# Kernel tuning notes

Hardware: AMD Instinct MI355X
Metric: run time of the kernel (lower is better)

## Reference

```python
import jax, jax.numpy as jnp
import numpy as np

VOCAB = 100000
BEO = 512
BATCH = 2048
SEQ = 50
MEAN = 0.0
STD = 1.0


def _linear_params(key, fan_in, fan_out):
    k1, k2 = jax.random.split(key)
    bound = 1.0 / np.sqrt(fan_in)
    W = jax.random.uniform(k1, (fan_in, fan_out), jnp.float32, -bound, bound)
    b = jax.random.uniform(k2, (fan_out,), jnp.float32, -bound, bound)
    return W, b


def setup_inputs() -> dict:
    key = jax.random.key(0)
    ks = jax.random.split(key, 8)
    s = jax.random.randint(ks[0], (BATCH, SEQ), 0, VOCAB, dtype=jnp.int64)
    x = jax.random.normal(ks[1], (BATCH, BEO), dtype=jnp.float32)
    W_bow_h, b_bow_h = _linear_params(ks[2], VOCAB, 256)
    W_bow_pred, b_bow_pred = _linear_params(ks[3], 256, 5)
    W_bow_embd, b_bow_embd = _linear_params(ks[4], 256, 64)
    W_beo_h, b_beo_h = _linear_params(ks[5], BEO, 256)
    W_beo_pred, b_beo_pred = _linear_params(ks[6], 256, 5)
    W_beo_embd, b_beo_embd = _linear_params(ks[7], 256, 64)
    return {
        "s": s, "x": x,
        "W_bow_h": W_bow_h, "b_bow_h": b_bow_h,
        "W_bow_pred": W_bow_pred, "b_bow_pred": b_bow_pred,
        "W_bow_embd": W_bow_embd, "b_bow_embd": b_bow_embd,
        "W_beo_h": W_beo_h, "b_beo_h": b_beo_h,
        "W_beo_pred": W_beo_pred, "b_beo_pred": b_beo_pred,
        "W_beo_embd": W_beo_embd, "b_beo_embd": b_beo_embd,
    }


def reference(s, x,
              W_bow_h, b_bow_h, W_bow_pred, b_bow_pred, W_bow_embd, b_bow_embd,
              W_beo_h, b_beo_h, W_beo_pred, b_beo_pred, W_beo_embd, b_beo_embd):
    B = s.shape[0]
    xn = (x - MEAN) / STD
    # multi-hot: scatter_ sets 1 regardless of duplicates (set, not add)
    rows = jnp.arange(B)[:, None]  # [B,1] broadcasts against s [B,SEQ]
    bow = jnp.zeros((B, VOCAB), jnp.float32).at[rows, s].set(1.0)
    bow_h = jax.nn.leaky_relu(bow @ W_bow_h + b_bow_h, 0.2)  # [B,256]
    beo_h = jax.nn.leaky_relu(xn @ W_beo_h + b_beo_h, 0.2)   # [B,256]
    bow_p = bow_h @ W_bow_pred + b_bow_pred  # [B,5]
    beo_p = beo_h @ W_beo_pred + b_beo_pred  # [B,5]
    bow_e = bow_h @ W_bow_embd + b_bow_embd  # [B,64]
    beo_e = beo_h @ W_beo_embd + b_beo_embd  # [B,64]
    return (bow_e, beo_e, bow_p, beo_p)
```

## Files before the change

### kernel.cpp

```cpp
#include <hip/hip_runtime.h>
#include <cstdint>

#define VOCAB 100000
#define NB    2048
#define SEQ   50
#define HID   256
#define XIN   512
#define NE    64
#define NP    5

#define BEO_BLOCKS 256
#define BEO_ROWS   8
#define NBLK (BEO_BLOCKS + NB)

#define OFF_BOW_E 0
#define OFF_BEO_E (NB*NE)
#define OFF_BOW_P (2*NB*NE)
#define OFF_BEO_P (2*NB*NE + NB*NP)

#define GITER 13

struct BeoS { float xs[BEO_ROWS][XIN]; };
struct BowS { float part[4*HID]; float h[HID]; };
union  SMem { BeoS beo; BowS bow; };

__global__ __launch_bounds__(256, 1) void fused_kernel(
    const int*   __restrict__ s,   const float* __restrict__ x,
    const float* __restrict__ Wbh, const float* __restrict__ bbh,
    const float* __restrict__ Wbp, const float* __restrict__ bbp,
    const float* __restrict__ Wbe, const float* __restrict__ bbe,
    const float* __restrict__ Weh, const float* __restrict__ beh,
    const float* __restrict__ Wep, const float* __restrict__ bep,
    const float* __restrict__ Wee, const float* __restrict__ bee,
    float* __restrict__ out)
{
    __shared__ SMem sm;
    const int tid = threadIdx.x;
    const int blk = blockIdx.x;

    if (blk < BEO_BLOCKS) {
        const int r0 = blk * BEO_ROWS;
        {
            const float4* src = (const float4*)(x + (size_t)r0 * XIN);
            float4*       dst = (float4*)&sm.beo.xs[0][0];
            #pragma unroll
            for (int i = 0; i < (BEO_ROWS*XIN/4)/256; ++i)
                dst[i*256 + tid] = src[i*256 + tid];
        }
        __syncthreads();

        float acc[BEO_ROWS];
        {
            float bv = beh[tid];
            #pragma unroll
            for (int r = 0; r < BEO_ROWS; ++r) acc[r] = bv;
        }
        const float4* xs4 = (const float4*)&sm.beo.xs[0][0];
        #pragma unroll 2
        for (int k4 = 0; k4 < XIN/4; ++k4) {
            const float* wcol = Weh + (size_t)(4*k4)*HID + tid;
            float w0 = wcol[0];
            float w1 = wcol[HID];
            float w2 = wcol[2*HID];
            float w3 = wcol[3*HID];
            #pragma unroll
            for (int r = 0; r < BEO_ROWS; ++r) {
                float4 xv = xs4[r*(XIN/4) + k4];
                acc[r] = fmaf(xv.x, w0, acc[r]);
                acc[r] = fmaf(xv.y, w1, acc[r]);
                acc[r] = fmaf(xv.z, w2, acc[r]);
                acc[r] = fmaf(xv.w, w3, acc[r]);
            }
        }
        __syncthreads();
        float* hs = &sm.beo.xs[0][0];
        #pragma unroll
        for (int r = 0; r < BEO_ROWS; ++r) {
            float v = acc[r];
            hs[r*HID + tid] = v > 0.f ? v : 0.2f*v;
        }
        __syncthreads();

        {
            const int jj = tid & 63;
            const int r  = tid >> 6;
            const float4* hs4 = (const float4*)hs;
            float s0 = 0.f, s1 = 0.f;
            #pragma unroll 4
            for (int k4 = 0; k4 < HID/4; ++k4) {
                float4 ha = hs4[r*(HID/4) + k4];
                float4 hb = hs4[(r+4)*(HID/4) + k4];
                const float* wp = Wee + (size_t)(4*k4)*NE + jj;
                float w0 = wp[0], w1 = wp[NE], w2 = wp[2*NE], w3 = wp[3*NE];
                s0 = fmaf(ha.x, w0, s0); s0 = fmaf(ha.y, w1, s0);
                s0 = fmaf(ha.z, w2, s0); s0 = fmaf(ha.w, w3, s0);
                s1 = fmaf(hb.x, w0, s1); s1 = fmaf(hb.y, w1, s1);
                s1 = fmaf(hb.z, w2, s1); s1 = fmaf(hb.w, w3, s1);
            }
            float bias = bee[jj];
            out[OFF_BEO_E + (size_t)(r0+r)*NE   + jj] = s0 + bias;
            out[OFF_BEO_E + (size_t)(r0+r+4)*NE + jj] = s1 + bias;
        }
        if (tid < BEO_ROWS*NP) {
            const int r = tid / NP, jj = tid % NP;
            float sp = bep[jj];
            for (int k = 0; k < HID; ++k)
                sp = fmaf(hs[r*HID + k], Wep[k*NP + jj], sp);
            out[OFF_BEO_P + (size_t)(r0+r)*NP + jj] = sp;
        }
    } else {
        const int row  = blk - BEO_BLOCKS;
        const int lane = tid & 63;
        const int w    = tid >> 6;
        const int* srow = s + row * SEQ;

        int tokl = (lane < SEQ) ? srow[lane] : -3;

        int   tk[GITER];
        float mk[GITER];
        #pragma unroll
        for (int ii = 0; ii < GITER; ++ii) {
            const int i = w + 4*ii;
            int t = (i < SEQ) ? srow[i] : -3;
            t = __builtin_amdgcn_readfirstlane(t);
            unsigned long long dup = __ballot(lane < i && tokl == t);
            mk[ii] = (t >= 0 && dup == 0ull) ? 1.0f : 0.0f;
            tk[ii] = (t < 0) ? 0 : t;
        }

        float4 v[GITER];
        const float* wbase = Wbh + (size_t)lane * 4;
        #pragma unroll
        for (int ii = 0; ii < GITER; ++ii)
            v[ii] = *(const float4*)(wbase + (size_t)tk[ii] * HID);
        __builtin_amdgcn_sched_barrier(0);

        float ax = 0.f, ay = 0.f, az = 0.f, aw = 0.f;
        #pragma unroll
        for (int ii = 0; ii < GITER; ++ii) {
            ax = fmaf(mk[ii], v[ii].x, ax);
            ay = fmaf(mk[ii], v[ii].y, ay);
            az = fmaf(mk[ii], v[ii].z, az);
            aw = fmaf(mk[ii], v[ii].w, aw);
        }
        *(float4*)&sm.bow.part[w*HID + lane*4] = make_float4(ax, ay, az, aw);
        __syncthreads();
        {
            float hv = sm.bow.part[tid] + sm.bow.part[HID + tid]
                     + sm.bow.part[2*HID + tid] + sm.bow.part[3*HID + tid]
                     + bbh[tid];
            hv = hv > 0.f ? hv : 0.2f*hv;
            sm.bow.h[tid] = hv;
        }
        __syncthreads();

        {
            const int jj = tid & 63, p = tid >> 6;
            const float4* h4 = (const float4*)sm.bow.h;
            float ps = 0.f;
            #pragma unroll 4
            for (int k4 = 0; k4 < 16; ++k4) {
                float4 hv = h4[p*16 + k4];
                const float* wp = Wbe + (size_t)(p*64 + 4*k4)*NE + jj;
                ps = fmaf(hv.x, wp[0],    ps);
                ps = fmaf(hv.y, wp[NE],   ps);
                ps = fmaf(hv.z, wp[2*NE], ps);
                ps = fmaf(hv.w, wp[3*NE], ps);
            }
            sm.bow.part[tid] = ps;
        }
        __syncthreads();
        float pp = 0.f;
        if (tid < 8*NP) {
            const int p = tid / NP, jj = tid % NP;
            #pragma unroll 8
            for (int kk = 0; kk < 32; ++kk) {
                int k = p*32 + kk;
                pp = fmaf(sm.bow.h[k], Wbp[k*NP + jj], pp);
            }
        }
        if (tid < NE) {
            float e = sm.bow.part[tid] + sm.bow.part[tid+64]
                    + sm.bow.part[tid+128] + sm.bow.part[tid+192] + bbe[tid];
            out[OFF_BOW_E + (size_t)row*NE + tid] = e;
        }
        __syncthreads();
        if (tid < 8*NP) sm.bow.part[tid] = pp;
        __syncthreads();
        if (tid < NP) {
            float sp = bbp[tid];
            #pragma unroll
            for (int q = 0; q < 8; ++q) sp += sm.bow.part[q*NP + tid];
            out[OFF_BOW_P + (size_t)row*NP + tid] = sp;
        }
    }
}

extern "C" void kernel_launch(void* const* d_in, const int* in_sizes, int n_in,
                              void* d_out, int out_size, void* d_ws, size_t ws_size,
                              hipStream_t stream) {
    const int*   s   = (const int*)  d_in[0];
    const float* x   = (const float*)d_in[1];
    const float* Wbh = (const float*)d_in[2];
    const float* bbh = (const float*)d_in[3];
    const float* Wbp = (const float*)d_in[4];
    const float* bbp = (const float*)d_in[5];
    const float* Wbe = (const float*)d_in[6];
    const float* bbe = (const float*)d_in[7];
    const float* Weh = (const float*)d_in[8];
    const float* beh = (const float*)d_in[9];
    const float* Wep = (const float*)d_in[10];
    const float* bep = (const float*)d_in[11];
    const float* Wee = (const float*)d_in[12];
    const float* bee = (const float*)d_in[13];

    fused_kernel<<<dim3(NBLK), dim3(256), 0, stream>>>(
        s, x, Wbh, bbh, Wbp, bbp, Wbe, bbe,
        Weh, beh, Wep, bep, Wee, bee, (float*)d_out);
}
```

Measured before the change: 215.2 us.

## Split fused kernel into separate bow and beo kernels with wider bow blocks

Splits the single fused kernel into two launches: a bag-of-words kernel using 1024-thread blocks (16 waves, 4 tokens each) and a separate dense beo kernel. Spreading each row's gather across more waves is meant to raise memory-level parallelism and shorten the per-row gather latency chain. The cost is an extra kernel launch, serialization of the two branches on the stream instead of running concurrently, and a larger shared-memory reduction.

```diff
diff --git a/kernel.cpp b/kernel.cpp
--- a/kernel.cpp
+++ b/kernel.cpp
@@ -9,190 +9,188 @@
 #define NE    64
 #define NP    5
 
-#define BEO_BLOCKS 256
-#define BEO_ROWS   8
-#define NBLK (BEO_BLOCKS + NB)
-
 #define OFF_BOW_E 0
 #define OFF_BEO_E (NB*NE)
 #define OFF_BOW_P (2*NB*NE)
 #define OFF_BEO_P (2*NB*NE + NB*NP)
 
-#define GITER 13
-
-struct BeoS { float xs[BEO_ROWS][XIN]; };
-struct BowS { float part[4*HID]; float h[HID]; };
-union  SMem { BeoS beo; BowS bow; };
-
-__global__ __launch_bounds__(256, 1) void fused_kernel(
-    const int*   __restrict__ s,   const float* __restrict__ x,
-    const float* __restrict__ Wbh, const float* __restrict__ bbh,
+#define BOW_T   1024
+#define BOW_W   16
+#define BOW_TPW 4
+
+__global__ __launch_bounds__(BOW_T, 4) void bow_kernel(
+    const int*   __restrict__ s,   const float* __restrict__ Wbh,
+    const float* __restrict__ bbh,
     const float* __restrict__ Wbp, const float* __restrict__ bbp,
     const float* __restrict__ Wbe, const float* __restrict__ bbe,
+    float* __restrict__ out)
+{
+    __shared__ float part[BOW_W*HID];
+    __shared__ float h[HID];
+    const int tid  = threadIdx.x;
+    const int row  = blockIdx.x;
+    const int lane = tid & 63;
+    const int w    = tid >> 6;
+    const int* srow = s + row*SEQ;
+
+    int tokl = (lane < SEQ) ? srow[lane] : -3;
+
+    int   tk[BOW_TPW];
+    float mk[BOW_TPW];
+    #pragma unroll
+    for (int ii = 0; ii < BOW_TPW; ++ii) {
+        const int i = w + BOW_W*ii;
+        int t = (i < SEQ) ? srow[i] : -3;
+        t = __builtin_amdgcn_readfirstlane(t);
+        unsigned long long dup = __ballot(lane < i && tokl == t);
+        mk[ii] = (t >= 0 && dup == 0ull) ? 1.0f : 0.0f;
+        tk[ii] = (t < 0) ? 0 : t;
+    }
+
+    float4 v[BOW_TPW];
+    const float* wbase = Wbh + (size_t)lane*4;
+    #pragma unroll
+    for (int ii = 0; ii < BOW_TPW; ++ii)
+        v[ii] = *(const float4*)(wbase + (size_t)tk[ii]*HID);
+    __builtin_amdgcn_sched_barrier(0);
+
+    float ax=0.f, ay=0.f, az=0.f, aw_=0.f;
+    #pragma unroll
+    for (int ii = 0; ii < BOW_TPW; ++ii) {
+        ax = fmaf(mk[ii], v[ii].x, ax);
+        ay = fmaf(mk[ii], v[ii].y, ay);
+        az = fmaf(mk[ii], v[ii].z, az);
+        aw_= fmaf(mk[ii], v[ii].w, aw_);
+    }
+    *(float4*)&part[w*HID + lane*4] = make_float4(ax, ay, az, aw_);
+    __syncthreads();
+
+    if (tid < HID) {
+        float hv = bbh[tid];
+        #pragma unroll
+        for (int p = 0; p < BOW_W; ++p) hv += part[p*HID + tid];
+        hv = hv > 0.f ? hv : 0.2f*hv;
+        h[tid] = hv;
+    }
+    __syncthreads();
+
+    {
+        const int jj = tid & 63, p2 = tid >> 6;
+        float ps = 0.f;
+        #pragma unroll
+        for (int kk = 0; kk < 16; ++kk) {
+            int k = p2*16 + kk;
+            ps = fmaf(h[k], Wbe[k*NE + jj], ps);
+        }
+        part[tid] = ps;
+    }
+    float pp = 0.f;
+    if (tid < 8*NP) {
+        const int p = tid / NP, jj = tid % NP;
+        #pragma unroll 8
+        for (int kk = 0; kk < 32; ++kk) {
+            int k = p*32 + kk;
+            pp = fmaf(h[k], Wbp[k*NP + jj], pp);
+        }
+    }
+    __syncthreads();
+    if (tid < NE) {
+        float e = bbe[tid];
+        #pragma unroll
+        for (int p2 = 0; p2 < 16; ++p2) e += part[p2*64 + tid];
+        out[OFF_BOW_E + (size_t)row*NE + tid] = e;
+    }
+    __syncthreads();
+    if (tid < 8*NP) part[tid] = pp;
+    __syncthreads();
+    if (tid < NP) {
+        float sp = bbp[tid];
+        #pragma unroll
+        for (int q = 0; q < 8; ++q) sp += part[q*NP + tid];
+        out[OFF_BOW_P + (size_t)row*NP + tid] = sp;
+    }
+}
+
+#define BEO_BLOCKS 256
+#define BEO_ROWS   8
+
+__global__ __launch_bounds__(256, 1) void beo_kernel(
+    const float* __restrict__ x,
     const float* __restrict__ Weh, const float* __restrict__ beh,
     const float* __restrict__ Wep, const float* __restrict__ bep,
     const float* __restrict__ Wee, const float* __restrict__ bee,
     float* __restrict__ out)
 {
-    __shared__ SMem sm;
+    __shared__ float xs[BEO_ROWS*XIN];
     const int tid = threadIdx.x;
-    const int blk = blockIdx.x;
-
-    if (blk < BEO_BLOCKS) {
-        const int r0 = blk * BEO_ROWS;
-        {
-            const float4* src = (const float4*)(x + (size_t)r0 * XIN);
-            float4*       dst = (float4*)&sm.beo.xs[0][0];
-            #pragma unroll
-            for (int i = 0; i < (BEO_ROWS*XIN/4)/256; ++i)
-                dst[i*256 + tid] = src[i*256 + tid];
-        }
-        __syncthreads();
-
-        float acc[BEO_ROWS];
-        {
-            float bv = beh[tid];
-            #pragma unroll
-            for (int r = 0; r < BEO_ROWS; ++r) acc[r] = bv;
-        }
-        const float4* xs4 = (const float4*)&sm.beo.xs[0][0];
-        #pragma unroll 2
-        for (int k4 = 0; k4 < XIN/4; ++k4) {
-            const float* wcol = Weh + (size_t)(4*k4)*HID + tid;
-            float w0 = wcol[0];
-            float w1 = wcol[HID];
-            float w2 = wcol[2*HID];
-            float w3 = wcol[3*HID];
-            #pragma unroll
-            for (int r = 0; r < BEO_ROWS; ++r) {
-                float4 xv = xs4[r*(XIN/4) + k4];
-                acc[r] = fmaf(xv.x, w0, acc[r]);
-                acc[r] = fmaf(xv.y, w1, acc[r]);
-                acc[r] = fmaf(xv.z, w2, acc[r]);
-                acc[r] = fmaf(xv.w, w3, acc[r]);
-            }
-        }
-        __syncthreads();
-        float* hs = &sm.beo.xs[0][0];
+    const int r0  = blockIdx.x * BEO_ROWS;
+    {
+        const float4* src = (const float4*)(x + (size_t)r0 * XIN);
+        float4*       dst = (float4*)xs;
+        #pragma unroll
+        for (int i = 0; i < (BEO_ROWS*XIN/4)/256; ++i)
+            dst[i*256 + tid] = src[i*256 + tid];
+    }
+    __syncthreads();
+
+    float acc[BEO_ROWS];
+    {
+        float bv = beh[tid];
+        #pragma unroll
+        for (int r = 0; r < BEO_ROWS; ++r) acc[r] = bv;
+    }
+    const float4* xs4 = (const float4*)xs;
+    #pragma unroll 2
+    for (int k4 = 0; k4 < XIN/4; ++k4) {
+        const float* wcol = Weh + (size_t)(4*k4)*HID + tid;
+        float w0 = wcol[0];
+        float w1 = wcol[HID];
+        float w2 = wcol[2*HID];
+        float w3 = wcol[3*HID];
         #pragma unroll
         for (int r = 0; r < BEO_ROWS; ++r) {
-            float v = acc[r];
-            hs[r*HID + tid] = v > 0.f ? v : 0.2f*v;
-        }
-        __syncthreads();
-
-        {
-            const int jj = tid & 63;
-            const int r  = tid >> 6;
-            const float4* hs4 = (const float4*)hs;
-            float s0 = 0.f, s1 = 0.f;
-            #pragma unroll 4
-            for (int k4 = 0; k4 < HID/4; ++k4) {
-                float4 ha = hs4[r*(HID/4) + k4];
-                float4 hb = hs4[(r+4)*(HID/4) + k4];
-                const float* wp = Wee + (size_t)(4*k4)*NE + jj;
-                float w0 = wp[0], w1 = wp[NE], w2 = wp[2*NE], w3 = wp[3*NE];
-                s0 = fmaf(ha.x, w0, s0); s0 = fmaf(ha.y, w1, s0);
-                s0 = fmaf(ha.z, w2, s0); s0 = fmaf(ha.w, w3, s0);
-                s1 = fmaf(hb.x, w0, s1); s1 = fmaf(hb.y, w1, s1);
-                s1 = fmaf(hb.z, w2, s1); s1 = fmaf(hb.w, w3, s1);
-            }
-            float bias = bee[jj];
-            out[OFF_BEO_E + (size_t)(r0+r)*NE   + jj] = s0 + bias;
-            out[OFF_BEO_E + (size_t)(r0+r+4)*NE + jj] = s1 + bias;
-        }
-        if (tid < BEO_ROWS*NP) {
-            const int r = tid / NP, jj = tid % NP;
-            float sp = bep[jj];
-            for (int k = 0; k < HID; ++k)
-                sp = fmaf(hs[r*HID + k], Wep[k*NP + jj], sp);
-            out[OFF_BEO_P + (size_t)(r0+r)*NP + jj] = sp;
-        }
-    } else {
-        const int row  = blk - BEO_BLOCKS;
-        const int lane = tid & 63;
-        const int w    = tid >> 6;
-        const int* srow = s + row * SEQ;
-
-        int tokl = (lane < SEQ) ? srow[lane] : -3;
-
-        int   tk[GITER];
-        float mk[GITER];
-        #pragma unroll
-        for (int ii = 0; ii < GITER; ++ii) {
-            const int i = w + 4*ii;
-            int t = (i < SEQ) ? srow[i] : -3;
-            t = __builtin_amdgcn_readfirstlane(t);
-            unsigned long long dup = __ballot(lane < i && tokl == t);
-            mk[ii] = (t >= 0 && dup == 0ull) ? 1.0f : 0.0f;
-            tk[ii] = (t < 0) ? 0 : t;
-        }
-
-        float4 v[GITER];
-        const float* wbase = Wbh + (size_t)lane * 4;
-        #pragma unroll
-        for (int ii = 0; ii < GITER; ++ii)
-            v[ii] = *(const float4*)(wbase + (size_t)tk[ii] * HID);
-        __builtin_amdgcn_sched_barrier(0);
-
-        float ax = 0.f, ay = 0.f, az = 0.f, aw = 0.f;
-        #pragma unroll
-        for (int ii = 0; ii < GITER; ++ii) {
-            ax = fmaf(mk[ii], v[ii].x, ax);
-            ay = fmaf(mk[ii], v[ii].y, ay);
-            az = fmaf(mk[ii], v[ii].z, az);
-            aw = fmaf(mk[ii], v[ii].w, aw);
-        }
-        *(float4*)&sm.bow.part[w*HID + lane*4] = make_float4(ax, ay, az, aw);
-        __syncthreads();
-        {
-            float hv = sm.bow.part[tid] + sm.bow.part[HID + tid]
-                     + sm.bow.part[2*HID + tid] + sm.bow.part[3*HID + tid]
-                     + bbh[tid];
-            hv = hv > 0.f ? hv : 0.2f*hv;
-            sm.bow.h[tid] = hv;
-        }
-        __syncthreads();
-
-        {
-            const int jj = tid & 63, p = tid >> 6;
-            const float4* h4 = (const float4*)sm.bow.h;
-            float ps = 0.f;
-            #pragma unroll 4
-            for (int k4 = 0; k4 < 16; ++k4) {
-                float4 hv = h4[p*16 + k4];
-                const float* wp = Wbe + (size_t)(p*64 + 4*k4)*NE + jj;
-                ps = fmaf(hv.x, wp[0],    ps);
-                ps = fmaf(hv.y, wp[NE],   ps);
-                ps = fmaf(hv.z, wp[2*NE], ps);
-                ps = fmaf(hv.w, wp[3*NE], ps);
-            }
-            sm.bow.part[tid] = ps;
-        }
-        __syncthreads();
-        float pp = 0.f;
-        if (tid < 8*NP) {
-            const int p = tid / NP, jj = tid % NP;
-            #pragma unroll 8
-            for (int kk = 0; kk < 32; ++kk) {
-                int k = p*32 + kk;
-                pp = fmaf(sm.bow.h[k], Wbp[k*NP + jj], pp);
-            }
-        }
-        if (tid < NE) {
-            float e = sm.bow.part[tid] + sm.bow.part[tid+64]
-                    + sm.bow.part[tid+128] + sm.bow.part[tid+192] + bbe[tid];
-            out[OFF_BOW_E + (size_t)row*NE + tid] = e;
-        }
-        __syncthreads();
-        if (tid < 8*NP) sm.bow.part[tid] = pp;
-        __syncthreads();
-        if (tid < NP) {
-            float sp = bbp[tid];
-            #pragma unroll
-            for (int q = 0; q < 8; ++q) sp += sm.bow.part[q*NP + tid];
-            out[OFF_BOW_P + (size_t)row*NP + tid] = sp;
-        }
+            float4 xv = xs4[r*(XIN/4) + k4];
+            acc[r] = fmaf(xv.x, w0, acc[r]);
+            acc[r] = fmaf(xv.y, w1, acc[r]);
+            acc[r] = fmaf(xv.z, w2, acc[r]);
+            acc[r] = fmaf(xv.w, w3, acc[r]);
+        }
+    }
+    __syncthreads();
+    float* hs = xs;
+    #pragma unroll
+    for (int r = 0; r < BEO_ROWS; ++r) {
+        float vv = acc[r];
+        hs[r*HID + tid] = vv > 0.f ? vv : 0.2f*vv;
+    }
+    __syncthreads();
+
+    {
+        const int jj = tid & 63;
+        const int r  = tid >> 6;
+        const float4* hs4 = (const float4*)hs;
+        float s0 = 0.f, s1 = 0.f;
+        #pragma unroll 4
+        for (int k4 = 0; k4 < HID/4; ++k4) {
+            float4 ha = hs4[r*(HID/4) + k4];
+            float4 hb = hs4[(r+4)*(HID/4) + k4];
+            const float* wp = Wee + (size_t)(4*k4)*NE + jj;
+            float w0 = wp[0], w1 = wp[NE], w2 = wp[2*NE], w3 = wp[3*NE];
+            s0 = fmaf(ha.x, w0, s0); s0 = fmaf(ha.y, w1, s0);
+            s0 = fmaf(ha.z, w2, s0); s0 = fmaf(ha.w, w3, s0);
+            s1 = fmaf(hb.x, w0, s1); s1 = fmaf(hb.y, w1, s1);
+            s1 = fmaf(hb.z, w2, s1); s1 = fmaf(hb.w, w3, s1);
+        }
+        float bias = bee[jj];
+        out[OFF_BEO_E + (size_t)(r0+r)*NE   + jj] = s0 + bias;
+        out[OFF_BEO_E + (size_t)(r0+r+4)*NE + jj] = s1 + bias;
+    }
+    if (tid < BEO_ROWS*NP) {
+        const int r = tid / NP, jj = tid % NP;
+        float sp = bep[jj];
+        for (int k = 0; k < HID; ++k)
+            sp = fmaf(hs[r*HID + k], Wep[k*NP + jj], sp);
+        out[OFF_BEO_P + (size_t)(r0+r)*NP + jj] = sp;
     }
 }
 
@@ -213,8 +211,10 @@
     const float* bep = (const float*)d_in[11];
     const float* Wee = (const float*)d_in[12];
     const float* bee = (const float*)d_in[13];
-
-    fused_kernel<<<dim3(NBLK), dim3(256), 0, stream>>>(
-        s, x, Wbh, bbh, Wbp, bbp, Wbe, bbe,
-        Weh, beh, Wep, bep, Wee, bee, (float*)d_out);
+    float* out = (float*)d_out;
+
+    bow_kernel<<<dim3(NB), dim3(BOW_T), 0, stream>>>(
+        s, Wbh, bbh, Wbp, bbp, Wbe, bbe, out);
+    beo_kernel<<<dim3(BEO_BLOCKS), dim3(256), 0, stream>>>(
+        x, Weh, beh, Wep, bep, Wee, bee, out);
 }
```

Result: slower. 241.3 us (+12.1%).
